# Kernel tuning notes

Measured on AMD Instinct MI355X. Metric: run time of the kernel, lower is better.

The kernel has to match this reference:

```python
import jax, jax.numpy as jnp
import numpy as np

# MambaLayer: LayerNorm(dim) -> Mamba(d_model=dim, d_state=64, d_conv=4, expand=2)
# dims
B_SZ, L_SEQ, D_MODEL = 1, 1024, 768
EXPAND, D_STATE, D_CONV = 2, 64, 4
D_INNER = EXPAND * D_MODEL          # 1536
DT_RANK = (D_MODEL + 15) // 16      # 48 (mamba default: ceil(d_model/16))
LN_EPS = 1e-5


def setup_inputs() -> dict:
    key = jax.random.key(0)
    ks = jax.random.split(key, 12)
    f32 = jnp.float32
    x = jax.random.normal(ks[0], (B_SZ, L_SEQ, D_MODEL), dtype=f32)
    # LayerNorm params
    ln_g = jnp.ones((D_MODEL,), f32)
    ln_b = jnp.zeros((D_MODEL,), f32)
    # in_proj: d_model -> 2*d_inner (x and gate z), bias=False
    W_in = jax.random.normal(ks[1], (D_MODEL, 2 * D_INNER), f32) / np.sqrt(D_MODEL)
    # depthwise causal conv1d, width d_conv, groups=d_inner
    conv_w = jax.random.normal(ks[2], (D_INNER, D_CONV), f32) * 0.1
    conv_b = jnp.zeros((D_INNER,), f32)
    # x_proj: d_inner -> dt_rank + 2*d_state, bias=False
    W_x = jax.random.normal(ks[3], (D_INNER, DT_RANK + 2 * D_STATE), f32) / np.sqrt(D_INNER)
    # dt_proj: dt_rank -> d_inner, with special bias init so softplus(bias) in [1e-3, 0.1]
    W_dt = jax.random.normal(ks[4], (DT_RANK, D_INNER), f32) / np.sqrt(DT_RANK)
    dt_init = jnp.exp(jax.random.uniform(ks[5], (D_INNER,), f32) * (np.log(0.1) - np.log(1e-3)) + np.log(1e-3))
    b_dt = dt_init + jnp.log(-jnp.expm1(-dt_init))  # inverse softplus
    # S4D-real init: A_log[d, n] = log(n+1)
    A_log = jnp.log(jnp.broadcast_to(jnp.arange(1, D_STATE + 1, dtype=f32), (D_INNER, D_STATE)))
    D_skip = jnp.ones((D_INNER,), f32)
    # out_proj: d_inner -> d_model, bias=False
    W_out = jax.random.normal(ks[6], (D_INNER, D_MODEL), f32) / np.sqrt(D_INNER)
    return {
        "x": x, "ln_g": ln_g, "ln_b": ln_b, "W_in": W_in,
        "conv_w": conv_w, "conv_b": conv_b, "W_x": W_x,
        "W_dt": W_dt, "b_dt": b_dt, "A_log": A_log, "D_skip": D_skip,
        "W_out": W_out,
    }


def _mamba_layer(x, ln_g, ln_b, W_in, conv_w, conv_b, W_x, W_dt, b_dt, A_log, D_skip, W_out):
    B, L, C = x.shape
    d_inner, d_conv = conv_w.shape
    d_state = A_log.shape[1]
    dt_rank = W_dt.shape[0]

    # ---- LayerNorm ----
    mu = x.mean(-1, keepdims=True)
    var = x.var(-1, keepdims=True)
    xn = (x - mu) * jax.lax.rsqrt(var + LN_EPS) * ln_g + ln_b

    # ---- in_proj -> (x, z) ----
    xz = xn @ W_in                              # (B, L, 2*d_inner)
    xi, z = xz[..., :d_inner], xz[..., d_inner:]

    # ---- causal depthwise conv1d + SiLU ----
    xp = jnp.pad(xi, ((0, 0), (d_conv - 1, 0), (0, 0)))
    xc = conv_b
    for k in range(d_conv):  # d_conv=4: tiny fixed unroll
        xc = xc + xp[:, k:k + L, :] * conv_w[:, k]
    xc = jax.nn.silu(xc)                        # (B, L, d_inner)

    # ---- input-dependent SSM params ----
    dbl = xc @ W_x                              # (B, L, dt_rank + 2*d_state)
    dt_raw = dbl[..., :dt_rank]
    Bm = dbl[..., dt_rank:dt_rank + d_state]    # (B, L, d_state)
    Cm = dbl[..., dt_rank + d_state:]           # (B, L, d_state)
    dt = jax.nn.softplus(dt_raw @ W_dt + b_dt)  # (B, L, d_inner)

    A = -jnp.exp(A_log)                         # (d_inner, d_state)
    dA = jnp.exp(dt[..., None] * A)             # (B, L, d_inner, d_state)
    dBx = dt[..., None] * Bm[:, :, None, :] * xc[..., None]

    # ---- selective scan: h_t = dA_t * h_{t-1} + dBx_t ; y_t = <h_t, C_t> ----
    def step(h, inp):
        dA_t, dBx_t, C_t = inp
        h = dA_t * h + dBx_t                    # (B, d_inner, d_state)
        y = jnp.einsum('bdn,bn->bd', h, C_t)
        return h, y

    h0 = jnp.zeros((B, d_inner, d_state), dtype=x.dtype)
    _, ys = jax.lax.scan(step, h0, (dA.swapaxes(0, 1), dBx.swapaxes(0, 1), Cm.swapaxes(0, 1)))
    y = ys.swapaxes(0, 1) + xc * D_skip         # (B, L, d_inner)

    # ---- gate and out_proj ----
    y = y * jax.nn.silu(z)
    return y @ W_out                            # (B, L, d_model)


def reference(x, ln_g, ln_b, W_in, conv_w, conv_b, W_x, W_dt, b_dt, A_log, D_skip, W_out):
    return _mamba_layer(x, ln_g, ln_b, W_in, conv_w, conv_b, W_x, W_dt, b_dt, A_log, D_skip, W_out)
```

## Files before the change

### kernel.cpp

```cpp
#include <hip/hip_runtime.h>
#include <hip/hip_bf16.h>
#include <math.h>

#define D_MODEL 768
#define D_INNER 1536
#define L_SEQ   1024
#define DT_RANK 48
#define D_STATE 64
#define NXZ     3072
#define NDBL    176
#define NCHUNK  16
#define QCH     64
#define LOG2E   1.4426950408889634f

typedef short  bfrag8 __attribute__((ext_vector_type(8)));
typedef float  f32x4  __attribute__((ext_vector_type(4)));

__device__ inline unsigned short bf_hi_u(float v) {
    __hip_bfloat16 h = __float2bfloat16(v);
    return *reinterpret_cast<unsigned short*>(&h);
}
__device__ inline float bf_to_f(unsigned short u) {
    __hip_bfloat16 h = *reinterpret_cast<__hip_bfloat16*>(&u);
    return __bfloat162float(h);
}

template<int SPLIT>
__global__ __launch_bounds__(256) void tconv_kernel(const float* __restrict__ src, int R, int C,
        int Cvalid, unsigned short* __restrict__ dhi, unsigned short* __restrict__ dlo) {
    __shared__ float tile[32][33];
    int tx = threadIdx.x & 31, ty = threadIdx.x >> 5;
    int c0 = blockIdx.x * 32, r0 = blockIdx.y * 32;
    #pragma unroll
    for (int i = 0; i < 4; i++) {
        int c = c0 + tx;
        tile[ty + 8*i][tx] = (c < Cvalid) ? src[(size_t)(r0 + ty + 8*i) * C + c] : 0.f;
    }
    __syncthreads();
    #pragma unroll
    for (int i = 0; i < 4; i++) {
        float v = tile[tx][ty + 8*i];
        size_t o = (size_t)(c0 + ty + 8*i) * R + r0 + tx;
        unsigned short h = bf_hi_u(v);
        dhi[o] = h;
        if (SPLIT) dlo[o] = bf_hi_u(v - bf_to_f(h));
    }
}

__global__ __launch_bounds__(256) void ln_kernel(const float* __restrict__ x,
        const float* __restrict__ g, const float* __restrict__ b,
        unsigned short* __restrict__ xn_hi, unsigned short* __restrict__ xn_lo) {
    int row = blockIdx.x;
    const float* xr = x + row * D_MODEL;
    float v[3];
    float s = 0.f, s2 = 0.f;
    #pragma unroll
    for (int i = 0; i < 3; i++) {
        v[i] = xr[threadIdx.x + i * 256];
        s += v[i]; s2 += v[i] * v[i];
    }
    #pragma unroll
    for (int o = 32; o > 0; o >>= 1) {
        s  += __shfl_xor(s,  o, 64);
        s2 += __shfl_xor(s2, o, 64);
    }
    __shared__ float red[2][4];
    int wid = threadIdx.x >> 6;
    if ((threadIdx.x & 63) == 0) { red[0][wid] = s; red[1][wid] = s2; }
    __syncthreads();
    s  = red[0][0] + red[0][1] + red[0][2] + red[0][3];
    s2 = red[1][0] + red[1][1] + red[1][2] + red[1][3];
    float mu  = s * (1.f / D_MODEL);
    float var = s2 * (1.f / D_MODEL) - mu * mu;
    float r   = rsqrtf(var + 1e-5f);
    #pragma unroll
    for (int i = 0; i < 3; i++) {
        int c = threadIdx.x + i * 256;
        float xv = (v[i] - mu) * r * g[c] + b[c];
        unsigned short h = bf_hi_u(xv);
        xn_hi[row * D_MODEL + c] = h;
        xn_lo[row * D_MODEL + c] = bf_hi_u(xv - bf_to_f(h));
    }
}

template<int BM, int SPLIT3, int ATOMIC>
__global__ __launch_bounds__(256, 2) void mgemm(
        const unsigned short* __restrict__ Ahi, const unsigned short* __restrict__ Alo,
        const unsigned short* __restrict__ Bhi, const unsigned short* __restrict__ Blo,
        float* __restrict__ C, int ldc, int K, int nvalid) {
    constexpr int NP = SPLIT3 ? 2 : 1;
    constexpr int MI = BM / 32;
    __shared__ unsigned short As[NP][BM][32];
    __shared__ unsigned short Bs[NP][128][32];
    int tid = threadIdx.x;
    int m0 = blockIdx.x * BM, n0 = blockIdx.y * 128;
    int nk = K / 32 / gridDim.z;
    int kbase = blockIdx.z * nk * 32;

    int i0 = tid,        i1 = tid + 256;
    int r0i = i0 >> 2,   k0i = (i0 & 3) * 8;
    int r1i = i1 >> 2,   k1i = (i1 & 3) * 8;
    int sc0 = k0i ^ (8 * (r0i & 3));
    int sc1 = k1i ^ (8 * (r1i & 3));

    const unsigned short* gA0h = Ahi + (size_t)(m0 + r0i) * K + kbase + k0i;
    const unsigned short* gA1h = (BM == 128) ? (Ahi + (size_t)(m0 + r1i) * K + kbase + k1i) : nullptr;
    const unsigned short* gB0h = Bhi + (size_t)(n0 + r0i) * K + kbase + k0i;
    const unsigned short* gB1h = Bhi + (size_t)(n0 + r1i) * K + kbase + k1i;
    const unsigned short* gA0l = SPLIT3 ? (Alo + (size_t)(m0 + r0i) * K + kbase + k0i) : nullptr;
    const unsigned short* gA1l = (SPLIT3 && BM == 128) ? (Alo + (size_t)(m0 + r1i) * K + kbase + k1i) : nullptr;
    const unsigned short* gB0l = SPLIT3 ? (Blo + (size_t)(n0 + r0i) * K + kbase + k0i) : nullptr;
    const unsigned short* gB1l = SPLIT3 ? (Blo + (size_t)(n0 + r1i) * K + kbase + k1i) : nullptr;

    uint4 va0h = *(const uint4*)gA0h;
    uint4 va1h; if (BM == 128) va1h = *(const uint4*)gA1h;
    uint4 vb0h = *(const uint4*)gB0h, vb1h = *(const uint4*)gB1h;
    uint4 va0l, va1l, vb0l, vb1l;
    if (SPLIT3) {
        va0l = *(const uint4*)gA0l;
        if (BM == 128) va1l = *(const uint4*)gA1l;
        vb0l = *(const uint4*)gB0l; vb1l = *(const uint4*)gB1l;
    }

    int wv = tid >> 6, L = tid & 63;
    int wr = (wv >> 1) * (MI * 16), wc = (wv & 1) * 64;
    int lm = L & 15, kq8 = (L >> 4) * 8;
    int rcol = kq8 ^ (8 * (L & 3));

    f32x4 acc[MI][4];
    #pragma unroll
    for (int i = 0; i < MI; i++)
        #pragma unroll
        for (int j = 0; j < 4; j++)
            #pragma unroll
            for (int r = 0; r < 4; r++) acc[i][j][r] = 0.f;

    for (int kt = 0; kt < nk; kt++) {
        __syncthreads();
        *(uint4*)&As[0][r0i][sc0] = va0h;
        if (BM == 128) *(uint4*)&As[0][r1i][sc1] = va1h;
        *(uint4*)&Bs[0][r0i][sc0] = vb0h;
        *(uint4*)&Bs[0][r1i][sc1] = vb1h;
        if (SPLIT3) {
            *(uint4*)&As[1][r0i][sc0] = va0l;
            if (BM == 128) *(uint4*)&As[1][r1i][sc1] = va1l;
            *(uint4*)&Bs[1][r0i][sc0] = vb0l;
            *(uint4*)&Bs[1][r1i][sc1] = vb1l;
        }
        __syncthreads();
        if (kt + 1 < nk) {
            int o = (kt + 1) * 32;
            va0h = *(const uint4*)(gA0h + o);
            if (BM == 128) va1h = *(const uint4*)(gA1h + o);
            vb0h = *(const uint4*)(gB0h + o); vb1h = *(const uint4*)(gB1h + o);
            if (SPLIT3) {
                va0l = *(const uint4*)(gA0l + o);
                if (BM == 128) va1l = *(const uint4*)(gA1l + o);
                vb0l = *(const uint4*)(gB0l + o); vb1l = *(const uint4*)(gB1l + o);
            }
        }
        bfrag8 fah[MI], fal[MI];
        #pragma unroll
        for (int mi = 0; mi < MI; mi++) {
            fah[mi] = *(const bfrag8*)&As[0][wr + mi * 16 + lm][rcol];
            if (SPLIT3) fal[mi] = *(const bfrag8*)&As[1][wr + mi * 16 + lm][rcol];
        }
        #pragma unroll
        for (int ni = 0; ni < 4; ni++) {
            bfrag8 fbh = *(const bfrag8*)&Bs[0][wc + ni * 16 + lm][rcol];
            #pragma unroll
            for (int mi = 0; mi < MI; mi++)
                acc[mi][ni] = __builtin_amdgcn_mfma_f32_16x16x32_bf16(fah[mi], fbh, acc[mi][ni], 0, 0, 0);
            if (SPLIT3) {
                bfrag8 fbl = *(const bfrag8*)&Bs[1][wc + ni * 16 + lm][rcol];
                #pragma unroll
                for (int mi = 0; mi < MI; mi++) {
                    acc[mi][ni] = __builtin_amdgcn_mfma_f32_16x16x32_bf16(fah[mi], fbl, acc[mi][ni], 0, 0, 0);
                    acc[mi][ni] = __builtin_amdgcn_mfma_f32_16x16x32_bf16(fal[mi], fbh, acc[mi][ni], 0, 0, 0);
                }
            }
        }
    }
    int rbase = (L >> 4) * 4, cbase = L & 15;
    #pragma unroll
    for (int mi = 0; mi < MI; mi++)
        #pragma unroll
        for (int ni = 0; ni < 4; ni++) {
            int cc = n0 + wc + ni * 16 + cbase;
            if (cc < nvalid) {
                #pragma unroll
                for (int r = 0; r < 4; r++) {
                    int rr = m0 + wr + mi * 16 + rbase + r;
                    if (ATOMIC) atomicAdd(&C[(size_t)rr * ldc + cc], acc[mi][ni][r]);
                    else        C[(size_t)rr * ldc + cc] = acc[mi][ni][r];
                }
            }
        }
}

template<int EPI, int TRANS>
__global__ __launch_bounds__(256) void gemm64(
        const float* __restrict__ A, int lda,
        const float* __restrict__ B, int ldb,
        float* __restrict__ C, int ldc,
        int N, int K, const float* __restrict__ bias) {
    __shared__ float As[16][68];
    __shared__ float Bs[16][68];
    int m0 = blockIdx.x * 64;
    int n0 = blockIdx.y * 64;
    int tid = threadIdx.x;
    int tx = tid & 15, ty = tid >> 4;
    int arow = tid >> 2, acol = (tid & 3) * 4;
    int brow = tid >> 4, bcol = (tid & 15) * 4;

    int nk = K / 16;

    const float* Aptr = A + (size_t)(m0 + arow) * lda + acol;
    const float* Bptr = B + (size_t)brow * ldb;

    float acc[4][4] = {};
    float4 av = *(const float4*)(Aptr);
    float4 bv = *(const float4*)(Bptr + n0 + bcol);

    for (int kt = 0; kt < nk; kt++) {
        __syncthreads();
        As[acol + 0][arow] = av.x;
        As[acol + 1][arow] = av.y;
        As[acol + 2][arow] = av.z;
        As[acol + 3][arow] = av.w;
        *(float4*)&Bs[brow][bcol] = bv;
        __syncthreads();
        if (kt + 1 < nk) {
            av = *(const float4*)(Aptr + (kt + 1) * 16);
            bv = *(const float4*)(Bptr + (size_t)(kt + 1) * 16 * ldb + n0 + bcol);
        }
        #pragma unroll
        for (int k = 0; k < 16; k++) {
            float4 a4 = *(const float4*)&As[k][ty * 4];
            float4 b4 = *(const float4*)&Bs[k][tx * 4];
            float ar[4] = {a4.x, a4.y, a4.z, a4.w};
            float br[4] = {b4.x, b4.y, b4.z, b4.w};
            #pragma unroll
            for (int i = 0; i < 4; i++)
                #pragma unroll
                for (int j = 0; j < 4; j++)
                    acc[i][j] = fmaf(ar[i], br[j], acc[i][j]);
        }
    }
    if (TRANS) {
        #pragma unroll
        for (int j = 0; j < 4; j++) {
            int col = n0 + tx * 4 + j;
            float4 v4;
            float* vp = (float*)&v4;
            #pragma unroll
            for (int i = 0; i < 4; i++) {
                float v = acc[i][j];
                if (EPI == 1) {
                    float u = v + bias[col];
                    v = (u > 15.f) ? u : log1pf(__expf(u));
                }
                vp[i] = v;
            }
            *(float4*)&C[(size_t)col * ldc + m0 + ty * 4] = v4;
        }
    } else {
        #pragma unroll
        for (int i = 0; i < 4; i++) {
            int row = m0 + ty * 4 + i;
            #pragma unroll
            for (int j = 0; j < 4; j++) {
                int col = n0 + tx * 4 + j;
                float v = acc[i][j];
                if (EPI == 1) {
                    float u = v + bias[col];
                    v = (u > 15.f) ? u : log1pf(__expf(u));
                }
                C[(size_t)row * ldc + col] = v;
            }
        }
    }
}

__global__ __launch_bounds__(256) void conv_t_kernel(const float* __restrict__ xz,
        const float* __restrict__ cw, const float* __restrict__ cb,
        float* __restrict__ xc_t, unsigned short* __restrict__ xcb_hi,
        unsigned short* __restrict__ xcb_lo) {
    __shared__ float tile[67][65];
    int d0 = blockIdx.x * 64, t0 = blockIdx.y * 64;
    int lane = threadIdx.x & 63, grp = threadIdx.x >> 6;
    #pragma unroll
    for (int p = 0; p < 17; p++) {
        int r = p * 4 + grp;
        if (r < 67) {
            int t = t0 - 3 + r;
            tile[r][lane] = (t >= 0) ? xz[(size_t)t * NXZ + d0 + lane] : 0.f;
        }
    }
    __syncthreads();
    #pragma unroll
    for (int p = 0; p < 16; p++) {
        int dl = grp + p * 4;
        int d = d0 + dl;
        float acc = cb[d];
        #pragma unroll
        for (int k = 0; k < 4; k++) acc = fmaf(tile[lane + k][dl], cw[d * 4 + k], acc);
        float s = acc / (1.f + __expf(-acc));
        xc_t[(size_t)d * L_SEQ + t0 + lane] = s;
    }
    #pragma unroll
    for (int p = 0; p < 16; p++) {
        int tl = grp + p * 4;
        int d = d0 + lane;
        float acc = cb[d];
        #pragma unroll
        for (int k = 0; k < 4; k++) acc = fmaf(tile[tl + k][lane], cw[d * 4 + k], acc);
        float s = acc / (1.f + __expf(-acc));
        unsigned short h = bf_hi_u(s);
        size_t o = (size_t)(t0 + tl) * D_INNER + d;
        xcb_hi[o] = h;
        xcb_lo[o] = bf_hi_u(s - bf_to_f(h));
    }
}

__global__ __launch_bounds__(256, 2) void scan_loc(
        const float* __restrict__ dt_t, const float* __restrict__ xc_t,
        const float* __restrict__ dbl, const float* __restrict__ A_log,
        const float* __restrict__ D_skip,
        float* __restrict__ y_t, float* __restrict__ hloc, float* __restrict__ sdt) {
    __shared__ float Bsh[QCH][64];
    __shared__ float Csh[QCH][64];
    __shared__ float dtsh[32][65];
    __shared__ float xcsh[32][65];
    int tid = threadIdx.x;
    int wid = tid >> 6, lane = tid & 63;
    int c = blockIdx.y, tbase = c * QCH;
    int d0blk = blockIdx.x * 32;
    int dl = wid * 8 + (lane >> 3);
    int d = d0blk + dl;
    int ng = lane & 7, n0 = ng * 8;

    #pragma unroll
    for (int j = 0; j < 16; j++) {
        int i = tid + j * 256;
        int tt = i >> 6, nn = i & 63;
        const float* row = dbl + (size_t)(tbase + tt) * NDBL + DT_RANK + nn;
        Bsh[tt][nn] = row[0];
        Csh[tt][nn] = row[D_STATE];
    }
    #pragma unroll
    for (int j = 0; j < 8; j++) {
        int i = tid + j * 256;
        int r = i >> 6, col = i & 63;
        dtsh[r][col] = dt_t[(size_t)(d0blk + r) * L_SEQ + tbase + col];
        xcsh[r][col] = xc_t[(size_t)(d0blk + r) * L_SEQ + tbase + col];
    }

    float np1 = (float)(n0 + 1);
    float Dv8 = D_skip[d] * 0.125f;
    float h0v = 0.f, h1v = 0.f, h2v = 0.f, h3v = 0.f;
    float h4v = 0.f, h5v = 0.f, h6v = 0.f, h7v = 0.f;
    float sdtv = 0.f;
    float* py = y_t + (size_t)d * L_SEQ + tbase + ng;
    __syncthreads();

#define SCAN_STEP(T, PDST)                                                    \
    {                                                                         \
        float dtv = dtsh[dl][T];                                              \
        float xcv = xcsh[dl][T];                                              \
        float4 b0 = *(const float4*)&Bsh[T][n0];                              \
        float4 b1 = *(const float4*)&Bsh[T][n0 + 4];                          \
        float4 c0 = *(const float4*)&Csh[T][n0];                              \
        float4 c1 = *(const float4*)&Csh[T][n0 + 4];                          \
        float m  = -LOG2E * dtv;                                              \
        float w  = __builtin_amdgcn_exp2f(m);                                 \
        float e0 = __builtin_amdgcn_exp2f(m * np1);                           \
        float w2 = w * w, w4 = w2 * w2;                                       \
        float a1 = e0 * w, a2 = e0 * w2, a3 = a1 * w2;                        \
        float a4 = e0 * w4, a5 = a1 * w4, a6 = a2 * w4, a7 = a3 * w4;         \
        float u = dtv * xcv;                                                  \
        h0v = fmaf(e0, h0v, u * b0.x); h1v = fmaf(a1, h1v, u * b0.y);         \
        h2v = fmaf(a2, h2v, u * b0.z); h3v = fmaf(a3, h3v, u * b0.w);         \
        h4v = fmaf(a4, h4v, u * b1.x); h5v = fmaf(a5, h5v, u * b1.y);         \
        h6v = fmaf(a6, h6v, u * b1.z); h7v = fmaf(a7, h7v, u * b1.w);         \
        float s0 = fmaf(h0v, c0.x, xcv * Dv8);                                \
        s0 = fmaf(h2v, c0.z, s0); s0 = fmaf(h4v, c1.x, s0);                   \
        s0 = fmaf(h6v, c1.z, s0);                                             \
        float s1 = h1v * c0.y;                                                \
        s1 = fmaf(h3v, c0.w, s1); s1 = fmaf(h5v, c1.y, s1);                   \
        s1 = fmaf(h7v, c1.w, s1);                                             \
        PDST = s0 + s1;                                                       \
        sdtv += dtv;                                                          \
    }

    #pragma unroll 1
    for (int g = 0; g < 8; g++) {
        int t0i = g * 8;
        float p0, p1, p2, p3, p4, p5, p6, p7;
        SCAN_STEP(t0i + 0, p0)
        SCAN_STEP(t0i + 1, p1)
        SCAN_STEP(t0i + 2, p2)
        SCAN_STEP(t0i + 3, p3)
        SCAN_STEP(t0i + 4, p4)
        SCAN_STEP(t0i + 5, p5)
        SCAN_STEP(t0i + 6, p6)
        SCAN_STEP(t0i + 7, p7)
        bool bb0 = (lane & 1) != 0;
        float q0 = (bb0 ? p1 : p0) + __shfl_xor(bb0 ? p0 : p1, 1, 64);
        float q1 = (bb0 ? p3 : p2) + __shfl_xor(bb0 ? p2 : p3, 1, 64);
        float q2 = (bb0 ? p5 : p4) + __shfl_xor(bb0 ? p4 : p5, 1, 64);
        float q3 = (bb0 ? p7 : p6) + __shfl_xor(bb0 ? p6 : p7, 1, 64);
        bool bb1 = (lane & 2) != 0;
        float r0v = (bb1 ? q1 : q0) + __shfl_xor(bb1 ? q0 : q1, 2, 64);
        float r1v = (bb1 ? q3 : q2) + __shfl_xor(bb1 ? q2 : q3, 2, 64);
        bool bb2 = (lane & 4) != 0;
        float sv = (bb2 ? r1v : r0v) + __shfl_xor(bb2 ? r0v : r1v, 4, 64);
        py[g * 8] = sv;
    }
#undef SCAN_STEP

    float4 ho0 = {h0v, h1v, h2v, h3v};
    float4 ho1 = {h4v, h5v, h6v, h7v};
    float* ph = hloc + ((size_t)(c * D_INNER + d)) * D_STATE + n0;
    *(float4*)ph = ho0;
    *(float4*)(ph + 4) = ho1;
    if (ng == 0) sdt[c * D_INNER + d] = sdtv;
}

__global__ __launch_bounds__(256) void scan_s2(
        const float* __restrict__ hloc, const float* __restrict__ sdt,
        const float* __restrict__ A_log, float* __restrict__ Hinit) {
    int idx = blockIdx.x * 256 + threadIdx.x;
    int d = idx >> 6;
    float An2 = -__expf(A_log[idx]) * LOG2E;
    float H = 0.f;
    #pragma unroll
    for (int c = 0; c < NCHUNK; c++) {
        int o = c * (D_INNER * D_STATE) + idx;
        Hinit[o] = H;
        H = fmaf(__builtin_amdgcn_exp2f(sdt[c * D_INNER + d] * An2), H, hloc[o]);
    }
}

__global__ __launch_bounds__(256, 4) void scan_corr_h(
        const float* __restrict__ dt_t, const float* __restrict__ dbl,
        const float* __restrict__ Hinit, const float* __restrict__ y_t,
        const float* __restrict__ xz, unsigned short* __restrict__ yb) {
    __shared__ float Cs[QCH][65];
    int tid = threadIdx.x;
    int wid = tid >> 6, lane = tid & 63;
    int c = blockIdx.y, tbase = c * QCH;
    int d = blockIdx.x * 4 + wid;
    #pragma unroll
    for (int j = 0; j < 16; j++) {
        int i = tid + j * 256;
        int tt = i >> 6, nn = i & 63;
        Cs[tt][nn] = dbl[(size_t)(tbase + tt) * NDBL + DT_RANK + D_STATE + nn];
    }
    float dt = dt_t[(size_t)d * L_SEQ + tbase + lane];
    float cum = dt;
    #pragma unroll
    for (int off = 1; off < 64; off <<= 1) {
        int src = (lane >= off) ? (lane - off) : lane;
        float v = __shfl(cum, src, 64);
        cum += (lane >= off) ? v : 0.f;
    }
    float rho = __builtin_amdgcn_exp2f(-LOG2E * cum);
    float hn = Hinit[((size_t)c * D_INNER + d) * D_STATE + lane];
    __syncthreads();
    float a3 = Cs[lane][63] * __shfl(hn, 63, 64);
    #pragma unroll
    for (int n = 62; n >= 48; n--)
        a3 = fmaf(a3, rho, Cs[lane][n] * __shfl(hn, n, 64));
    float a2 = Cs[lane][47] * __shfl(hn, 47, 64);
    #pragma unroll
    for (int n = 46; n >= 32; n--)
        a2 = fmaf(a2, rho, Cs[lane][n] * __shfl(hn, n, 64));
    float a1 = Cs[lane][31] * __shfl(hn, 31, 64);
    #pragma unroll
    for (int n = 30; n >= 16; n--)
        a1 = fmaf(a1, rho, Cs[lane][n] * __shfl(hn, n, 64));
    float a0 = Cs[lane][15] * __shfl(hn, 15, 64);
    #pragma unroll
    for (int n = 14; n >= 0; n--)
        a0 = fmaf(a0, rho, Cs[lane][n] * __shfl(hn, n, 64));
    float r2  = rho * rho;
    float r4  = r2 * r2;
    float r8  = r4 * r4;
    float r16 = r8 * r8;
    float acc = fmaf(a3, r16, a2);
    acc = fmaf(acc, r16, a1);
    acc = fmaf(acc, r16, a0);
    float corr = acc * rho;
    float yl = y_t[(size_t)d * L_SEQ + tbase + lane];
    float zv = xz[(size_t)(tbase + lane) * NXZ + D_INNER + d];
    float yv = corr + yl;
    yb[(size_t)(tbase + lane) * D_INNER + d] = bf_hi_u(yv * (zv / (1.f + __expf(-zv))));
}

extern "C" void kernel_launch(void* const* d_in, const int* in_sizes, int n_in,
                              void* d_out, int out_size, void* d_ws, size_t ws_size,
                              hipStream_t stream) {
    const float* x      = (const float*)d_in[0];
    const float* ln_g   = (const float*)d_in[1];
    const float* ln_b   = (const float*)d_in[2];
    const float* W_in   = (const float*)d_in[3];
    const float* conv_w = (const float*)d_in[4];
    const float* conv_b = (const float*)d_in[5];
    const float* W_x    = (const float*)d_in[6];
    const float* W_dt   = (const float*)d_in[7];
    const float* b_dt   = (const float*)d_in[8];
    const float* A_log  = (const float*)d_in[9];
    const float* D_skip = (const float*)d_in[10];
    const float* W_out  = (const float*)d_in[11];

    float* ws   = (float*)d_ws;
    float* xz   = ws;
    float* xc_t = ws + 3145728;
    float* dbl  = ws + 4718592;
    float* dt_t = ws + 4898816;
    float* hloc = ws + 6471680;
    float* Hini = ws + 8044544;
    float* sdt  = ws + 9617408;
    unsigned short* ubase     = (unsigned short*)(ws + 9641984);
    unsigned short* xn_hi     = ubase;
    unsigned short* xn_lo     = ubase + 786432;
    unsigned short* yv_b      = ubase;
    unsigned short* Wt_in_hi  = ubase + 1572864;
    unsigned short* Wt_in_lo  = ubase + 3932160;
    unsigned short* Wt_out_hi = ubase + 6291456;
    unsigned short* WxT_hi    = ubase + 7471104;
    unsigned short* WxT_lo    = ubase + 7864320;
    unsigned short* xcb_hi    = ubase + 8257536;
    unsigned short* xcb_lo    = ubase + 9830400;
    float* y_t = (float*)xcb_hi;

    hipMemsetAsync(dbl, 0, (size_t)L_SEQ * NDBL * sizeof(float), stream);
    hipMemsetAsync(d_out, 0, (size_t)L_SEQ * D_MODEL * sizeof(float), stream);

    tconv_kernel<1><<<dim3(NXZ / 32, D_MODEL / 32), 256, 0, stream>>>(W_in, D_MODEL, NXZ, NXZ, Wt_in_hi, Wt_in_lo);
    tconv_kernel<0><<<dim3(D_MODEL / 32, D_INNER / 32), 256, 0, stream>>>(W_out, D_INNER, D_MODEL, D_MODEL, Wt_out_hi, nullptr);
    tconv_kernel<1><<<dim3(256 / 32, D_INNER / 32), 256, 0, stream>>>(W_x, D_INNER, NDBL, NDBL, WxT_hi, WxT_lo);

    ln_kernel<<<L_SEQ, 256, 0, stream>>>(x, ln_g, ln_b, xn_hi, xn_lo);
    mgemm<64, 1, 0><<<dim3(16, 24, 1), 256, 0, stream>>>(xn_hi, xn_lo, Wt_in_hi, Wt_in_lo, xz, NXZ, D_MODEL, NXZ);
    conv_t_kernel<<<dim3(D_INNER / 64, L_SEQ / 64), 256, 0, stream>>>(xz, conv_w, conv_b, xc_t, xcb_hi, xcb_lo);
    mgemm<128, 1, 1><<<dim3(8, 2, 16), 256, 0, stream>>>(xcb_hi, xcb_lo, WxT_hi, WxT_lo, dbl, NDBL, D_INNER, NDBL);
    gemm64<1, 1><<<dim3(16, 24, 1), 256, 0, stream>>>(dbl, NDBL, W_dt, D_INNER, dt_t, L_SEQ, D_INNER, DT_RANK, b_dt);
    scan_loc<<<dim3(D_INNER / 32, NCHUNK), 256, 0, stream>>>(dt_t, xc_t, dbl, A_log, D_skip, y_t, hloc, sdt);
    scan_s2<<<(D_INNER * D_STATE) / 256, 256, 0, stream>>>(hloc, sdt, A_log, Hini);
    scan_corr_h<<<dim3(D_INNER / 4, NCHUNK), 256, 0, stream>>>(dt_t, dbl, Hini, y_t, xz, yv_b);
    mgemm<64, 0, 1><<<dim3(16, 6, 4), 256, 0, stream>>>(yv_b, nullptr, Wt_out_hi, nullptr, (float*)d_out, D_MODEL, D_INNER, D_MODEL);
}
```

Measured before the change: 231.7 us.

## Merge weight transposes and LayerNorm into one kernel; split-K in_proj into two buffers

The three weight transpose/bf16-split kernels and the LayerNorm kernel are merged into a single launch that picks its role from the block index, saving three launches. The in_proj GEMM moves from BM=64 tiles to BM=128 tiles with split-K over two z slices. Each slice writes its partial sum to its own buffer, and the conv and gating kernels add the two partials when they read them. This keeps the parallelism the larger tile would otherwise lose, avoids atomics, and needs no memset of the output. The cost is an extra 12MB partial buffer, double the global reads of xz in the consumer kernels, and a new workspace offset that must fit inside the allocation.

```diff
diff --git a/kernel.cpp b/kernel.cpp
--- a/kernel.cpp
+++ b/kernel.cpp
@@ -26,11 +26,12 @@
 }
 
 template<int SPLIT>
-__global__ __launch_bounds__(256) void tconv_kernel(const float* __restrict__ src, int R, int C,
-        int Cvalid, unsigned short* __restrict__ dhi, unsigned short* __restrict__ dlo) {
+__device__ inline void tconv_body(const float* __restrict__ src, int R, int C,
+        int Cvalid, unsigned short* __restrict__ dhi, unsigned short* __restrict__ dlo,
+        int bx, int by, int tid) {
     __shared__ float tile[32][33];
-    int tx = threadIdx.x & 31, ty = threadIdx.x >> 5;
-    int c0 = blockIdx.x * 32, r0 = blockIdx.y * 32;
+    int tx = tid & 31, ty = tid >> 5;
+    int c0 = bx * 32, r0 = by * 32;
     #pragma unroll
     for (int i = 0; i < 4; i++) {
         int c = c0 + tx;
@@ -47,16 +48,16 @@
     }
 }
 
-__global__ __launch_bounds__(256) void ln_kernel(const float* __restrict__ x,
+__device__ inline void ln_body(const float* __restrict__ x,
         const float* __restrict__ g, const float* __restrict__ b,
-        unsigned short* __restrict__ xn_hi, unsigned short* __restrict__ xn_lo) {
-    int row = blockIdx.x;
+        unsigned short* __restrict__ xn_hi, unsigned short* __restrict__ xn_lo,
+        int row, int tid) {
     const float* xr = x + row * D_MODEL;
     float v[3];
     float s = 0.f, s2 = 0.f;
     #pragma unroll
     for (int i = 0; i < 3; i++) {
-        v[i] = xr[threadIdx.x + i * 256];
+        v[i] = xr[tid + i * 256];
         s += v[i]; s2 += v[i] * v[i];
     }
     #pragma unroll
@@ -65,8 +66,8 @@
         s2 += __shfl_xor(s2, o, 64);
     }
     __shared__ float red[2][4];
-    int wid = threadIdx.x >> 6;
-    if ((threadIdx.x & 63) == 0) { red[0][wid] = s; red[1][wid] = s2; }
+    int wid = tid >> 6;
+    if ((tid & 63) == 0) { red[0][wid] = s; red[1][wid] = s2; }
     __syncthreads();
     s  = red[0][0] + red[0][1] + red[0][2] + red[0][3];
     s2 = red[1][0] + red[1][1] + red[1][2] + red[1][3];
@@ -75,7 +76,7 @@
     float r   = rsqrtf(var + 1e-5f);
     #pragma unroll
     for (int i = 0; i < 3; i++) {
-        int c = threadIdx.x + i * 256;
+        int c = tid + i * 256;
         float xv = (v[i] - mu) * r * g[c] + b[c];
         unsigned short h = bf_hi_u(xv);
         xn_hi[row * D_MODEL + c] = h;
@@ -83,11 +84,39 @@
     }
 }
 
+#define NB_WIN  2304
+#define NB_WOUT 1152
+#define NB_WX   384
+#define NB_LN   1024
+
+__global__ __launch_bounds__(256) void prep_kernel(
+        const float* __restrict__ W_in, unsigned short* __restrict__ Wt_in_hi,
+        unsigned short* __restrict__ Wt_in_lo,
+        const float* __restrict__ W_out, unsigned short* __restrict__ Wt_out_hi,
+        const float* __restrict__ W_x, unsigned short* __restrict__ WxT_hi,
+        unsigned short* __restrict__ WxT_lo,
+        const float* __restrict__ x, const float* __restrict__ ln_g,
+        const float* __restrict__ ln_b,
+        unsigned short* __restrict__ xn_hi, unsigned short* __restrict__ xn_lo) {
+    int bid = blockIdx.x, tid = threadIdx.x;
+    if (bid < NB_WIN) {
+        tconv_body<1>(W_in, D_MODEL, NXZ, NXZ, Wt_in_hi, Wt_in_lo, bid % 96, bid / 96, tid);
+    } else if (bid < NB_WIN + NB_WOUT) {
+        int l = bid - NB_WIN;
+        tconv_body<0>(W_out, D_INNER, D_MODEL, D_MODEL, Wt_out_hi, nullptr, l % 24, l / 24, tid);
+    } else if (bid < NB_WIN + NB_WOUT + NB_WX) {
+        int l = bid - NB_WIN - NB_WOUT;
+        tconv_body<1>(W_x, D_INNER, NDBL, NDBL, WxT_hi, WxT_lo, l % 8, l / 8, tid);
+    } else {
+        ln_body(x, ln_g, ln_b, xn_hi, xn_lo, bid - NB_WIN - NB_WOUT - NB_WX, tid);
+    }
+}
+
 template<int BM, int SPLIT3, int ATOMIC>
 __global__ __launch_bounds__(256, 2) void mgemm(
         const unsigned short* __restrict__ Ahi, const unsigned short* __restrict__ Alo,
         const unsigned short* __restrict__ Bhi, const unsigned short* __restrict__ Blo,
-        float* __restrict__ C, int ldc, int K, int nvalid) {
+        float* __restrict__ C, int ldc, int K, int nvalid, size_t zoff) {
     constexpr int NP = SPLIT3 ? 2 : 1;
     constexpr int MI = BM / 32;
     __shared__ unsigned short As[NP][BM][32];
@@ -96,6 +125,7 @@
     int m0 = blockIdx.x * BM, n0 = blockIdx.y * 128;
     int nk = K / 32 / gridDim.z;
     int kbase = blockIdx.z * nk * 32;
+    C += (size_t)blockIdx.z * zoff;
 
     int i0 = tid,        i1 = tid + 256;
     int r0i = i0 >> 2,   k0i = (i0 & 3) * 8;
@@ -282,7 +312,8 @@
     }
 }
 
-__global__ __launch_bounds__(256) void conv_t_kernel(const float* __restrict__ xz,
+__global__ __launch_bounds__(256) void conv_t_kernel(const float* __restrict__ xza,
+        const float* __restrict__ xzb,
         const float* __restrict__ cw, const float* __restrict__ cb,
         float* __restrict__ xc_t, unsigned short* __restrict__ xcb_hi,
         unsigned short* __restrict__ xcb_lo) {
@@ -294,7 +325,8 @@
         int r = p * 4 + grp;
         if (r < 67) {
             int t = t0 - 3 + r;
-            tile[r][lane] = (t >= 0) ? xz[(size_t)t * NXZ + d0 + lane] : 0.f;
+            size_t o = (size_t)t * NXZ + d0 + lane;
+            tile[r][lane] = (t >= 0) ? (xza[o] + xzb[o]) : 0.f;
         }
     }
     __syncthreads();
@@ -445,7 +477,8 @@
 __global__ __launch_bounds__(256, 4) void scan_corr_h(
         const float* __restrict__ dt_t, const float* __restrict__ dbl,
         const float* __restrict__ Hinit, const float* __restrict__ y_t,
-        const float* __restrict__ xz, unsigned short* __restrict__ yb) {
+        const float* __restrict__ xza, const float* __restrict__ xzb,
+        unsigned short* __restrict__ yb) {
     __shared__ float Cs[QCH][65];
     int tid = threadIdx.x;
     int wid = tid >> 6, lane = tid & 63;
@@ -493,7 +526,8 @@
     acc = fmaf(acc, r16, a0);
     float corr = acc * rho;
     float yl = y_t[(size_t)d * L_SEQ + tbase + lane];
-    float zv = xz[(size_t)(tbase + lane) * NXZ + D_INNER + d];
+    size_t zo = (size_t)(tbase + lane) * NXZ + D_INNER + d;
+    float zv = xza[zo] + xzb[zo];
     float yv = corr + yl;
     yb[(size_t)(tbase + lane) * D_INNER + d] = bf_hi_u(yv * (zv / (1.f + __expf(-zv))));
 }
@@ -533,22 +567,22 @@
     unsigned short* WxT_lo    = ubase + 7864320;
     unsigned short* xcb_hi    = ubase + 8257536;
     unsigned short* xcb_lo    = ubase + 9830400;
+    float* xz2 = (float*)(ubase + 11403264);
     float* y_t = (float*)xcb_hi;
 
     hipMemsetAsync(dbl, 0, (size_t)L_SEQ * NDBL * sizeof(float), stream);
     hipMemsetAsync(d_out, 0, (size_t)L_SEQ * D_MODEL * sizeof(float), stream);
 
-    tconv_kernel<1><<<dim3(NXZ / 32, D_MODEL / 32), 256, 0, stream>>>(W_in, D_MODEL, NXZ, NXZ, Wt_in_hi, Wt_in_lo);
-    tconv_kernel<0><<<dim3(D_MODEL / 32, D_INNER / 32), 256, 0, stream>>>(W_out, D_INNER, D_MODEL, D_MODEL, Wt_out_hi, nullptr);
-    tconv_kernel<1><<<dim3(256 / 32, D_INNER / 32), 256, 0, stream>>>(W_x, D_INNER, NDBL, NDBL, WxT_hi, WxT_lo);
-
-    ln_kernel<<<L_SEQ, 256, 0, stream>>>(x, ln_g, ln_b, xn_hi, xn_lo);
-    mgemm<64, 1, 0><<<dim3(16, 24, 1), 256, 0, stream>>>(xn_hi, xn_lo, Wt_in_hi, Wt_in_lo, xz, NXZ, D_MODEL, NXZ);
-    conv_t_kernel<<<dim3(D_INNER / 64, L_SEQ / 64), 256, 0, stream>>>(xz, conv_w, conv_b, xc_t, xcb_hi, xcb_lo);
-    mgemm<128, 1, 1><<<dim3(8, 2, 16), 256, 0, stream>>>(xcb_hi, xcb_lo, WxT_hi, WxT_lo, dbl, NDBL, D_INNER, NDBL);
+    prep_kernel<<<NB_WIN + NB_WOUT + NB_WX + NB_LN, 256, 0, stream>>>(
+        W_in, Wt_in_hi, Wt_in_lo, W_out, Wt_out_hi, W_x, WxT_hi, WxT_lo,
+        x, ln_g, ln_b, xn_hi, xn_lo);
+    mgemm<128, 1, 0><<<dim3(8, 24, 2), 256, 0, stream>>>(
+        xn_hi, xn_lo, Wt_in_hi, Wt_in_lo, xz, NXZ, D_MODEL, NXZ, (size_t)L_SEQ * NXZ * 0 + (size_t)(xz2 - xz));
+    conv_t_kernel<<<dim3(D_INNER / 64, L_SEQ / 64), 256, 0, stream>>>(xz, xz2, conv_w, conv_b, xc_t, xcb_hi, xcb_lo);
+    mgemm<128, 1, 1><<<dim3(8, 2, 16), 256, 0, stream>>>(xcb_hi, xcb_lo, WxT_hi, WxT_lo, dbl, NDBL, D_INNER, NDBL, 0);
     gemm64<1, 1><<<dim3(16, 24, 1), 256, 0, stream>>>(dbl, NDBL, W_dt, D_INNER, dt_t, L_SEQ, D_INNER, DT_RANK, b_dt);
     scan_loc<<<dim3(D_INNER / 32, NCHUNK), 256, 0, stream>>>(dt_t, xc_t, dbl, A_log, D_skip, y_t, hloc, sdt);
     scan_s2<<<(D_INNER * D_STATE) / 256, 256, 0, stream>>>(hloc, sdt, A_log, Hini);
-    scan_corr_h<<<dim3(D_INNER / 4, NCHUNK), 256, 0, stream>>>(dt_t, dbl, Hini, y_t, xz, yv_b);
-    mgemm<64, 0, 1><<<dim3(16, 6, 4), 256, 0, stream>>>(yv_b, nullptr, Wt_out_hi, nullptr, (float*)d_out, D_MODEL, D_INNER, D_MODEL);
-}
+    scan_corr_h<<<dim3(D_INNER / 4, NCHUNK), 256, 0, stream>>>(dt_t, dbl, Hini, y_t, xz, xz2, yv_b);
+    mgemm<64, 0, 1><<<dim3(16, 6, 4), 256, 0, stream>>>(yv_b, nullptr, Wt_out_hi, nullptr, (float*)d_out, D_MODEL, D_INNER, D_MODEL, 0);
+}
```

New measurement: 228.5 us. Within noise of the previous version (-1.4%).
